# Performance work log

Hardware: AMD Instinct MI355X
Metric: run time of the kernel (lower is better)

Reference implementation:

```python
import jax, jax.numpy as jnp
import numpy as np
import math

N_FUNC = 32
LR_START, LR_DECAY = 1.0, 0.977
WEIGHT_DECAY, AMP_DECAY, MM_LR = 0.01, 0.01, 0.03
N_SAMP, BATCH, MOMENTUM = 32, 16, 0.85
N_FEAT, N_TARGET, MEM_SIZE = 1024, 512, 16384
DATA_SIZE = 100
SQRT_NF = math.sqrt(N_FUNC)


def setup_inputs() -> dict:
    key = jax.random.key(0)
    ks = jax.random.split(key, 16)
    p = jnp.linspace(0.01, 0.99, N_FUNC)[:, None]
    center_freq = jnp.log(p / (1.0 - p))  # logit of linspace, as in __init__
    return {
        "t": DATA_SIZE,
        "data_size": DATA_SIZE,
        "ts": jax.random.randint(ks[0], (N_SAMP,), 0, DATA_SIZE + 1),
        "x": jax.random.normal(ks[1], (N_FEAT,), jnp.float32),
        "z": jax.random.normal(ks[2], (N_TARGET,), jnp.float32),
        "memory": jax.random.normal(ks[3], (MEM_SIZE, N_TARGET), jnp.float32),
        "t_memory": jax.random.randint(ks[4], (MEM_SIZE,), 0, DATA_SIZE),
        "feat_memory": jax.random.normal(ks[5], (MEM_SIZE, N_FEAT), jnp.float32),
        "amp_re": 1.0 / SQRT_NF + 0.01 * jax.random.normal(ks[6], (N_FUNC, N_TARGET), jnp.float32),
        "amp_im": 0.01 * jax.random.normal(ks[7], (N_FUNC, N_TARGET), jnp.float32),
        "freq": 0.1 * jax.random.normal(ks[8], (N_FUNC, 1), jnp.float32),
        "center_freq": center_freq.astype(jnp.float32),
        "res_proj": 0.02 * jax.random.normal(ks[9], (N_FEAT + N_TARGET, N_TARGET), jnp.float32),
        "feat_mean": 0.1 * jax.random.normal(ks[10], (N_FEAT,), jnp.float32),
        "bias": 0.1 * jax.random.normal(ks[11], (N_TARGET,), jnp.float32),
        "amp_grad_re": 0.01 * jax.random.normal(ks[12], (N_FUNC, N_TARGET), jnp.float32),
        "amp_grad_im": 0.01 * jax.random.normal(ks[13], (N_FUNC, N_TARGET), jnp.float32),
        "freq_grad": 0.01 * jax.random.normal(ks[14], (N_FUNC, 1), jnp.float32),
        "res_proj_grad": 0.001 * jax.random.normal(ks[15], (N_FEAT + N_TARGET, N_TARGET), jnp.float32),
    }


def _get_freq(freq, center_freq):
    fr = center_freq + jnp.tanh(freq) * (64.0 / N_FUNC)
    return jax.nn.sigmoid(fr) * 0.5


def _evaluate(t, amp_re, amp_im, freq, bias, center_freq):
    # t: [B]; amp: [F, T]; freq/center_freq: [F, 1]
    fr = _get_freq(freq, center_freq)                      # [F, 1]
    ph = (2.0 * math.pi) * t[:, None, None] * fr           # [B, F, 1]
    # Re(exp(i*ph) * (amp_re + i*amp_im)) = cos*amp_re - sin*amp_im
    z = (jnp.cos(ph) * amp_re - jnp.sin(ph) * amp_im).sum(1) / SQRT_NF
    return z + bias                                        # [B, T]


def _get_resid(x, z, res_proj, feat_mean, bias):
    r = jnp.concatenate([x - feat_mean, z - bias], axis=-1) @ res_proj
    return r / (jnp.abs(r) + 1.0)


def reference(t, data_size, ts, x, z, memory, t_memory, feat_memory,
              amp_re, amp_im, freq, center_freq, res_proj, feat_mean, bias,
              amp_grad_re, amp_grad_im, freq_grad, res_proj_grad):
    # scatter new sample into the ring buffers
    memory = memory.at[data_size].set(z)
    feat_memory = feat_memory.at[data_size].set(x)
    t_memory = t_memory.at[data_size].set(t)
    ds_new = data_size + 1
    lr = LR_START * LR_DECAY ** ds_new  # lr after this call's decay
    # running means (torch uses the already-incremented data_size)
    bias = (bias * ds_new + z) / (ds_new + 1)
    feat_mean = (feat_mean * ds_new + x) / (ds_new + 1)

    for b in range(N_SAMP // BATCH):
        batch = ts[b * BATCH:(b + 1) * BATCH]
        t_b = t_memory[batch].astype(jnp.float32)
        z_b = memory[batch]
        x_b = feat_memory[batch]

        def loss_fn(a_re, a_im, fq, rp):
            z_ = _evaluate(t_b, a_re, a_im, fq, bias, center_freq)
            amp_abs = jnp.sqrt(a_re ** 2 + a_im ** 2)
            loss = jnp.sqrt(amp_abs).sum() * AMP_DECAY
            loss = loss + jnp.abs(z_b - z_).sum(-1).mean()
            resid = _get_resid(x_b, z_, rp, feat_mean, bias)
            z2 = jax.lax.stop_gradient(z_) + resid
            res_loss = jnp.abs(z_b - z2).sum(-1).mean()
            # torch uses self.res_proj (buffer) here -> no grad through this term
            res_loss = res_loss + jnp.abs(jax.lax.stop_gradient(rp)).sum() * WEIGHT_DECAY
            return loss + res_loss * MM_LR

        ag_re, ag_im, fg, rg = jax.grad(loss_fn, argnums=(0, 1, 2, 3))(amp_re, amp_im, freq, res_proj)
        # momentum decay then normalized-grad accumulate, then SGD step
        anorm = jnp.sqrt((ag_re ** 2).sum() + (ag_im ** 2).sum()) + 1.0  # complex vector norm
        amp_grad_re = amp_grad_re * MOMENTUM + ag_re / anorm
        amp_grad_im = amp_grad_im * MOMENTUM + ag_im / anorm
        amp_re = amp_re - amp_grad_re * lr
        amp_im = amp_im - amp_grad_im * lr
        fnorm = jnp.sqrt((fg ** 2).sum()) + 1.0
        freq_grad = freq_grad * MOMENTUM + fg / fnorm
        freq = freq - freq_grad * lr
        rnorm = jnp.sqrt((rg ** 2).sum()) + 1.0
        res_proj_grad = res_proj_grad * MOMENTUM + rg / rnorm
        res_proj = res_proj - res_proj_grad * lr

    return (memory, t_memory, feat_memory, amp_re, amp_im, freq, res_proj,
            bias, feat_mean, amp_grad_re, amp_grad_im, freq_grad, res_proj_grad)
```

## Files before the change

### kernel.cpp

```cpp
#include <hip/hip_runtime.h>
#include <hip/hip_cooperative_groups.h>
#include <math.h>

namespace cg = cooperative_groups;

#define NT 512
#define NF 1024
#define NFUNC 32
#define BATCHSZ 16

typedef float v4f __attribute__((ext_vector_type(4)));
typedef int   v4i __attribute__((ext_vector_type(4)));

constexpr int O_MEM  = 0;
constexpr int O_TMEM = 8388608;
constexpr int O_FEAT = 8404992;
constexpr int O_ARE  = 25182208;
constexpr int O_AIM  = 25198592;
constexpr int O_FREQ = 25214976;
constexpr int O_RP   = 25215008;
constexpr int O_BIAS = 26001440;
constexpr int O_FM   = 26001952;
constexpr int O_AGR  = 26002976;
constexpr int O_AGI  = 26019360;
constexpr int O_FGR  = 26035744;
constexpr int O_RPG  = 26035776;

constexpr int W_LR    = 0;
constexpr int W_ANORM = 2;
constexpr int W_RNORM = 4;
constexpr int W_GFR   = 8;
constexpr int W_TB    = 72;
constexpr int W_C     = 96;
constexpr int W_S     = 608;
constexpr int W_CATZ  = 1120;
constexpr int W_CATX  = 9312;
constexpr int W_GR    = 25696;
constexpr int W_G     = 33888;
constexpr int W_AGRE  = 42080;
constexpr int W_AGIM  = 58464;
constexpr int W_RPART = 74848;

constexpr float MM_LR = 0.03f;
constexpr float AMP_DECAY = 0.01f;
constexpr float MOM = 0.85f;
constexpr float INV_SQRT_NF = 0.17677669529663687f;
constexpr float TWO_PI = 6.283185307179586f;

constexpr int NB = 512;
constexpr int CHUNK = 786944;
constexpr int NCOPY = 256;

constexpr int R_MEM_END  = 2097152;
constexpr int R_FEAT_END = 6291456;

struct KParams {
    const int *t, *dsp, *ts;
    const float *x, *z, *memory;
    const int *t_memory;
    const float *feat_memory;
    const float *amp_re, *amp_im, *freq, *cf, *res_proj, *feat_mean, *bias;
    const float *amp_grad_re, *amp_grad_im, *freq_grad, *res_proj_grad;
    float *out, *ws;
};

__device__ __forceinline__ float sgnf(float x) {
    return (x > 0.f) ? 1.f : ((x < 0.f) ? -1.f : 0.f);
}

__device__ __forceinline__ float wave_reduce(float v) {
#pragma unroll
    for (int o = 32; o > 0; o >>= 1) v += __shfl_down(v, o, 64);
    return v;
}

__device__ __forceinline__ void copy_span(int tg, int nthr, int cbase, int cend,
    int dsv, int tt,
    const float* __restrict__ x, const float* __restrict__ z,
    const float* __restrict__ memory, const int* __restrict__ t_memory,
    const float* __restrict__ feat_memory, float* __restrict__ out)
{
    {
        const int a1 = cend < R_MEM_END ? cend : R_MEM_END;
        const v4f* __restrict__ src = (const v4f*)memory;
        const v4f* __restrict__ zz  = (const v4f*)z;
        v4f* __restrict__ dst = (v4f*)(out + O_MEM);
        int u = cbase + tg;
        for (; u + nthr < a1; u += 2 * nthr) {
            const int u1 = u + nthr;
            v4f v0 = __builtin_nontemporal_load((u  >> 7) == dsv ? zz + (u  & 127) : src + u );
            v4f v1 = __builtin_nontemporal_load((u1 >> 7) == dsv ? zz + (u1 & 127) : src + u1);
            __builtin_nontemporal_store(v0, dst + u );
            __builtin_nontemporal_store(v1, dst + u1);
        }
        for (; u < a1; u += nthr) {
            v4f v = __builtin_nontemporal_load((u >> 7) == dsv ? zz + (u & 127) : src + u);
            __builtin_nontemporal_store(v, dst + u);
        }
    }
    {
        const int a0 = cbase > R_MEM_END ? cbase : R_MEM_END;
        const int a1 = cend < R_FEAT_END ? cend : R_FEAT_END;
        const v4f* __restrict__ src = (const v4f*)feat_memory;
        const v4f* __restrict__ xx  = (const v4f*)x;
        v4f* __restrict__ dst = (v4f*)(out + O_FEAT);
        int u = a0 + tg;
        for (; u + nthr < a1; u += 2 * nthr) {
            const int u1 = u + nthr;
            const int f0 = u - R_MEM_END, f1 = u1 - R_MEM_END;
            v4f v0 = __builtin_nontemporal_load((f0 >> 8) == dsv ? xx + (f0 & 255) : src + f0);
            v4f v1 = __builtin_nontemporal_load((f1 >> 8) == dsv ? xx + (f1 & 255) : src + f1);
            __builtin_nontemporal_store(v0, dst + f0);
            __builtin_nontemporal_store(v1, dst + f1);
        }
        for (; u < a1; u += nthr) {
            const int f = u - R_MEM_END;
            v4f v = __builtin_nontemporal_load((f >> 8) == dsv ? xx + (f & 255) : src + f);
            __builtin_nontemporal_store(v, dst + f);
        }
    }
    {
        const int a0 = cbase > R_FEAT_END ? cbase : R_FEAT_END;
        const int a1 = cend;
        if (a1 > a0) {
            const float ft = (float)tt;
            const v4i* __restrict__ tm = (const v4i*)t_memory;
            v4f* __restrict__ dst = (v4f*)(out + O_TMEM);
            for (int u = a0 + tg; u < a1; u += nthr) {
                const int f = u - R_FEAT_END;
                const v4i iv = __builtin_nontemporal_load(tm + f);
                const int e = f * 4;
                v4f v;
                v.x = (e + 0 == dsv) ? ft : (float)iv.x;
                v.y = (e + 1 == dsv) ? ft : (float)iv.y;
                v.z = (e + 2 == dsv) ? ft : (float)iv.z;
                v.w = (e + 3 == dsv) ? ft : (float)iv.w;
                __builtin_nontemporal_store(v, dst + f);
            }
        }
    }
}

__global__ __launch_bounds__(256, 2) void k_fused(KParams p)
{
    cg::grid_group grid = cg::this_grid();
    const int bidx = (int)blockIdx.x;
    const int tid  = (int)threadIdx.x;

    __shared__ float c_l[32], s_l[32], cat[96];
    __shared__ float g_sh[NT], d_sh[NT];
    __shared__ float red[4];

    float* __restrict__ out = p.out;
    float* __restrict__ ws  = p.ws;
    const int dsv = *p.dsp;
    const int tt  = *p.t;
    const float nn = (float)(dsv + 1), dd = (float)(dsv + 2);
    const int tg   = bidx * 256 + tid;
    const int nthr = NB * 256;

    for (int b = 0; b < 2; ++b) {
        const float* __restrict__ are_src = b ? out + O_ARE : p.amp_re;
        const float* __restrict__ aim_src = b ? out + O_AIM : p.amp_im;
        const float* __restrict__ fq_src  = b ? out + O_FREQ: p.freq;
        const float* __restrict__ rp_src  = b ? out + O_RP  : p.res_proj;
        const float* __restrict__ agr_src = b ? out + O_AGR : p.amp_grad_re;
        const float* __restrict__ agi_src = b ? out + O_AGI : p.amp_grad_im;
        const float* __restrict__ fgr_src = b ? out + O_FGR : p.freq_grad;
        const float* __restrict__ rpg_src = b ? out + O_RPG : p.res_proj_grad;

        if (bidx < 256) {
            const int i = bidx >> 4, s = bidx & 15;
            const int bi = p.ts[b * BATCHSZ + i];
            if (tid < 32) {
                float f  = fq_src[tid];
                float th = tanhf(f);
                float u  = p.cf[tid] + 2.f * th;
                float sg = 1.f / (1.f + expf(-u));
                float fr = 0.5f * sg;
                float tb = (bi == dsv) ? (float)tt : (float)p.t_memory[bi];
                float ph = TWO_PI * tb * fr;
                float cv = cosf(ph), sv = sinf(ph);
                c_l[tid] = cv; s_l[tid] = sv;
                if (s == 0) {
                    ws[W_C + i*32 + tid] = cv; ws[W_S + i*32 + tid] = sv;
                    if (tid == 0) ws[W_TB + i] = tb;
                }
            }
            if (bidx == 0) {
                if (tid == 64) ws[W_ANORM + b] = 0.f;
                if (tid == 65) ws[W_RNORM + b] = 0.f;
                if (tid == 66 && b == 0) ws[W_LR] = (float)pow(0.977, (double)(dsv + 1));
                if (tid >= 96 && tid < 128) ws[W_GFR + b*32 + tid - 96] = 0.f;
            }
            __syncthreads();
            if (tid < 96) {
                int pe = s * 96 + tid;
                float cv;
                if (pe < NF) {
                    float fmv = (p.feat_mean[pe] * nn + p.x[pe]) / dd;
                    float xv  = (bi == dsv) ? p.x[pe] : p.feat_memory[bi*NF + pe];
                    cv = xv - fmv;
                    ws[W_CATX + i*NF + pe] = cv;
                } else {
                    int q = pe - NF;
                    float acc = 0.f;
#pragma unroll
                    for (int k = 0; k < 32; ++k)
                        acc += c_l[k] * are_src[k*NT + q] - s_l[k] * aim_src[k*NT + q];
                    cv = acc * INV_SQRT_NF;
                    ws[W_CATZ + i*NT + q] = cv;
                }
                cat[tid] = cv;
            }
            __syncthreads();
            const int j = tid;
            const float* rpb = rp_src + (size_t)s * 96 * NT;
            float a0 = 0.f, a1 = 0.f, b0 = 0.f, b1 = 0.f;
#pragma unroll 8
            for (int pp = 0; pp < 96; pp += 2) {
                float c0 = cat[pp], c1 = cat[pp + 1];
                a0 += c0 * rpb[pp*NT + j];
                a1 += c0 * rpb[pp*NT + j + 256];
                b0 += c1 * rpb[(pp+1)*NT + j];
                b1 += c1 * rpb[(pp+1)*NT + j + 256];
            }
            ws[W_RPART + s*8192 + i*NT + j]       = a0 + b0;
            ws[W_RPART + s*8192 + i*NT + j + 256] = a1 + b1;
        }
        {
            int cb = (b*4 + 0) * CHUNK;
            copy_span(tg, nthr, cb, cb + CHUNK, dsv, tt, p.x, p.z, p.memory, p.t_memory, p.feat_memory, out);
        }
        __threadfence();
        grid.sync();
        __threadfence();

        for (int vb = bidx; vb < 1024; vb += NB) {
            const int i = vb >> 6, jg = vb & 63;
            const int bi = p.ts[b * BATCHSZ + i];
#pragma unroll
            for (int ll = 0; ll < 2; ++ll) {
                int l = tid + ll * 256;
                float r = 0.f;
#pragma unroll
                for (int s = 0; s < 16; ++s) r += ws[W_RPART + s*8192 + i*NT + l];
                float bn = (p.bias[l] * nn + p.z[l]) / dd;
                float zj = ws[W_CATZ + i*NT + l] + bn;
                float zb = (bi == dsv) ? p.z[l] : p.memory[bi*NT + l];
                float s1 = sgnf(zj - zb);
                float ar = fabsf(r) + 1.f;
                float z2 = zj + r / ar;
                float g  = sgnf(z2 - zb) * (MM_LR / 16.f) / (ar * ar);
                g_sh[l] = g; d_sh[l] = s1 * (1.f / 16.f);
                if (jg == 0) {
                    ws[W_GR + i*NT + l] = g;
                    if (b == 0 && i == 0) out[O_BIAS + l] = bn;
                }
            }
            if (b == 0 && jg == 0 && i < 2) {
#pragma unroll
                for (int ll = 0; ll < 2; ++ll) {
                    int pe = i * 512 + tid + ll * 256;
                    out[O_FM + pe] = (p.feat_mean[pe] * nn + p.x[pe]) / dd;
                }
            }
            __syncthreads();
            const int w = tid >> 6, lane = tid & 63;
#pragma unroll
            for (int jj = 0; jj < 2; ++jj) {
                int j = jg * 8 + w * 2 + jj;
                const float* rrow = rp_src + (size_t)(NF + j) * NT;
                float acc = 0.f;
#pragma unroll
                for (int l = lane; l < NT; l += 64) acc += g_sh[l] * rrow[l];
                acc = wave_reduce(acc);
                if (lane == 0) ws[W_G + i*NT + j] = d_sh[j] + acc;
            }
            __syncthreads();
        }
        {
            int cb = (b*4 + 1) * CHUNK;
            copy_span(tg, nthr, cb, cb + CHUNK, dsv, tt, p.x, p.z, p.memory, p.t_memory, p.feat_memory, out);
        }
        __threadfence();
        grid.sync();
        __threadfence();

        for (int it = bidx; it < 3264; it += NB) {
            if (it < 64) {
                int e = it*256 + tid;
                int k = e >> 9;
                float gre = 0.f, gim = 0.f;
#pragma unroll
                for (int i2 = 0; i2 < 16; ++i2) {
                    float G = ws[W_G + i2*NT + (e & 511)];
                    gre += G * ws[W_C + i2*32 + k];
                    gim += G * ws[W_S + i2*32 + k];
                }
                float re = are_src[e], im = aim_src[e];
                float aa = sqrtf(re*re + im*im);
                float dec = AMP_DECAY / (2.f * aa * sqrtf(aa));
                float agr =  gre * INV_SQRT_NF + re * dec;
                float agi = -gim * INV_SQRT_NF + im * dec;
                ws[W_AGRE + e] = agr;
                ws[W_AGIM + e] = agi;
                float v = wave_reduce(agr*agr + agi*agi);
                if ((tid & 63) == 0) red[tid >> 6] = v;
                __syncthreads();
                if (tid == 0) atomicAdd(&ws[W_ANORM + b], red[0]+red[1]+red[2]+red[3]);
            } else if (it < 192) {
                int wid = tid >> 6, lane = tid & 63;
                int pair = (it - 64)*4 + wid;
                int i = pair >> 5, k = pair & 31;
                float ck = ws[W_C + i*32 + k], sk = ws[W_S + i*32 + k];
                float acc = 0.f;
#pragma unroll
                for (int j = lane; j < NT; j += 64)
                    acc += ws[W_G + i*NT + j] * (-sk * are_src[k*NT + j] - ck * aim_src[k*NT + j]);
                acc = wave_reduce(acc);
                if (lane == 0)
                    atomicAdd(&ws[W_GFR + b*32 + k], acc * TWO_PI * ws[W_TB + i] * INV_SQRT_NF);
            } else {
                int e = (it - 192)*256 + tid;
                int pr = e >> 9, j = e & 511;
                float rg = 0.f;
#pragma unroll
                for (int i2 = 0; i2 < 16; ++i2) {
                    float cv = (pr < NF) ? ws[W_CATX + i2*NF + pr]
                                         : ws[W_CATZ + i2*NT + (pr - NF)];
                    rg += cv * ws[W_GR + i2*NT + j];
                }
                float v = wave_reduce(rg * rg);
                if ((tid & 63) == 0) red[tid >> 6] = v;
                __syncthreads();
                if (tid == 0) atomicAdd(&ws[W_RNORM + b], red[0]+red[1]+red[2]+red[3]);
            }
            __syncthreads();
        }
        {
            int cb = (b*4 + 2) * CHUNK;
            copy_span(tg, nthr, cb, cb + CHUNK, dsv, tt, p.x, p.z, p.memory, p.t_memory, p.feat_memory, out);
        }
        __threadfence();
        grid.sync();
        __threadfence();

        const float lr = ws[W_LR];
        for (int it = bidx; it < 3137; it += NB) {
            if (it < 64) {
                int e = it*256 + tid;
                float anorm = sqrtf(ws[W_ANORM + b]) + 1.f;
                float mr = agr_src[e]*MOM + ws[W_AGRE + e]/anorm;
                out[O_AGR + e] = mr; out[O_ARE + e] = are_src[e] - mr*lr;
                float mi = agi_src[e]*MOM + ws[W_AGIM + e]/anorm;
                out[O_AGI + e] = mi; out[O_AIM + e] = aim_src[e] - mi*lr;
            } else if (it == 64) {
                if (tid < 64) {
                    float fg = 0.f, th = 0.f;
                    if (tid < 32) {
                        float f = fq_src[tid];
                        th = tanhf(f);
                        float u  = p.cf[tid] + 2.f*th;
                        float sg = 1.f / (1.f + expf(-u));
                        fg = ws[W_GFR + b*32 + tid] * sg*(1.f-sg)*(1.f-th*th);
                    }
                    float t2 = fg*fg;
#pragma unroll
                    for (int o = 32; o > 0; o >>= 1) t2 += __shfl_down(t2, o, 64);
                    float tot = __shfl(t2, 0, 64);
                    if (tid < 32) {
                        float fnorm = sqrtf(tot) + 1.f;
                        float m = fgr_src[tid]*MOM + fg/fnorm;
                        out[O_FGR + tid] = m;
                        out[O_FREQ + tid] = fq_src[tid] - m*lr;
                    }
                }
            } else {
                int e = (it - 65)*256 + tid;
                int pr = e >> 9, j = e & 511;
                float rg = 0.f;
#pragma unroll
                for (int i2 = 0; i2 < 16; ++i2) {
                    float cv = (pr < NF) ? ws[W_CATX + i2*NF + pr]
                                         : ws[W_CATZ + i2*NT + (pr - NF)];
                    rg += cv * ws[W_GR + i2*NT + j];
                }
                float rnorm = sqrtf(ws[W_RNORM + b]) + 1.f;
                float m = rpg_src[e]*MOM + rg/rnorm;
                out[O_RPG + e] = m; out[O_RP + e] = rp_src[e] - m*lr;
            }
        }
        {
            int cb = (b*4 + 3) * CHUNK;
            copy_span(tg, nthr, cb, cb + CHUNK, dsv, tt, p.x, p.z, p.memory, p.t_memory, p.feat_memory, out);
        }
        if (b == 0) { __threadfence(); grid.sync(); __threadfence(); }
    }
}

__device__ __forceinline__ void copy_role(int rb, int cbase, int ccnt,
    const int* __restrict__ tptr, const int* __restrict__ dsptr,
    const float* __restrict__ x, const float* __restrict__ z,
    const float* __restrict__ memory, const int* __restrict__ t_memory,
    const float* __restrict__ feat_memory, float* __restrict__ out)
{
    const int dsv = *dsptr;
    const int tt  = *tptr;
    copy_span(rb * 256 + (int)threadIdx.x, NCOPY * 256, cbase, cbase + ccnt,
              dsv, tt, x, z, memory, t_memory, feat_memory, out);
}

#define COPY_ARGS const int* __restrict__ tptr, const int* __restrict__ dsptr,            \
                  const float* __restrict__ x, const float* __restrict__ z,               \
                  const float* __restrict__ memory, const int* __restrict__ t_memory,     \
                  const float* __restrict__ feat_memory, int cbase, int ccnt
#define COPY_PASS tptr, dsptr, x, z, memory, t_memory, feat_memory

__global__ __launch_bounds__(256) void k_fwd_ab(int b, const int* __restrict__ ts,
    const float* __restrict__ cf,
    const float* __restrict__ are_src, const float* __restrict__ aim_src,
    const float* __restrict__ fq_src, const float* __restrict__ fm_in,
    const float* __restrict__ rp_src,
    float* __restrict__ out, float* __restrict__ ws, COPY_ARGS)
{
    int bb = blockIdx.x;
    const int tid = threadIdx.x;
    if (bb < NCOPY) { copy_role(bb, cbase, ccnt, COPY_PASS, out); return; }
    bb -= NCOPY;
    const int i = bb >> 4, s = bb & 15;
    __shared__ float c_l[32], s_l[32], cat[96];
    const int dsv = *dsptr;
    const int bi = ts[b * BATCHSZ + i];
    if (tid < 32) {
        float f  = fq_src[tid];
        float th = tanhf(f);
        float u  = cf[tid] + 2.f * th;
        float sg = 1.f / (1.f + expf(-u));
        float fr = 0.5f * sg;
        float tb = (bi == dsv) ? (float)(*tptr) : (float)t_memory[bi];
        float ph = TWO_PI * tb * fr;
        float cv = cosf(ph), sv = sinf(ph);
        c_l[tid] = cv; s_l[tid] = sv;
        if (s == 0) {
            ws[W_C + i*32 + tid] = cv; ws[W_S + i*32 + tid] = sv;
            if (tid == 0) ws[W_TB + i] = tb;
        }
    }
    if (bb == 0) {
        if (tid == 64) ws[W_ANORM + b] = 0.f;
        if (tid == 65) ws[W_RNORM + b] = 0.f;
        if (tid == 66 && b == 0) ws[W_LR] = (float)pow(0.977, (double)(dsv + 1));
        if (tid >= 96 && tid < 128) ws[W_GFR + b*32 + tid - 96] = 0.f;
    }
    __syncthreads();
    if (tid < 96) {
        int p = s * 96 + tid;
        float cv;
        if (p < NF) {
            const float nn = (float)(dsv + 1), dd = (float)(dsv + 2);
            float fmv = (fm_in[p] * nn + x[p]) / dd;
            float xv  = (bi == dsv) ? x[p] : feat_memory[bi*NF + p];
            cv = xv - fmv;
            ws[W_CATX + i*NF + p] = cv;
        } else {
            int q = p - NF;
            float acc = 0.f;
#pragma unroll
            for (int k = 0; k < 32; ++k)
                acc += c_l[k] * are_src[k*NT + q] - s_l[k] * aim_src[k*NT + q];
            cv = acc * INV_SQRT_NF;
            ws[W_CATZ + i*NT + q] = cv;
        }
        cat[tid] = cv;
    }
    __syncthreads();
    const int j = tid;
    const float* rpb = rp_src + (size_t)s * 96 * NT;
    float a0 = 0.f, a1 = 0.f, b0 = 0.f, b1 = 0.f;
#pragma unroll 8
    for (int p = 0; p < 96; p += 2) {
        float c0 = cat[p], c1 = cat[p + 1];
        a0 += c0 * rpb[p*NT + j];
        a1 += c0 * rpb[p*NT + j + 256];
        b0 += c1 * rpb[(p+1)*NT + j];
        b1 += c1 * rpb[(p+1)*NT + j + 256];
    }
    ws[W_RPART + s*8192 + i*NT + j]       = a0 + b0;
    ws[W_RPART + s*8192 + i*NT + j + 256] = a1 + b1;
}

__global__ __launch_bounds__(256) void k_eplg3(int b, const int* __restrict__ ts,
    const float* __restrict__ bias_in, const float* __restrict__ fm_in,
    const float* __restrict__ rp_src,
    float* __restrict__ out, float* __restrict__ ws, COPY_ARGS)
{
    int bb = blockIdx.x;
    const int tid = threadIdx.x;
    if (bb < NCOPY) { copy_role(bb, cbase, ccnt, COPY_PASS, out); return; }
    bb -= NCOPY;
    const int i = bb >> 6, jg = bb & 63;
    __shared__ float g_sh[NT], d_sh[NT];
    const int dsv = *dsptr;
    const int bi = ts[b * BATCHSZ + i];
    const float nn = (float)(dsv + 1), dd = (float)(dsv + 2);
#pragma unroll
    for (int ll = 0; ll < 2; ++ll) {
        int l = tid + ll * 256;
        float r = 0.f;
#pragma unroll
        for (int s = 0; s < 16; ++s) r += ws[W_RPART + s*8192 + i*NT + l];
        float bn = (bias_in[l] * nn + z[l]) / dd;
        float zj = ws[W_CATZ + i*NT + l] + bn;
        float zb = (bi == dsv) ? z[l] : memory[bi*NT + l];
        float s1 = sgnf(zj - zb);
        float ar = fabsf(r) + 1.f;
        float z2 = zj + r / ar;
        float g  = sgnf(z2 - zb) * (MM_LR / 16.f) / (ar * ar);
        g_sh[l] = g; d_sh[l] = s1 * (1.f / 16.f);
        if (jg == 0) {
            ws[W_GR + i*NT + l] = g;
            if (b == 0 && i == 0) out[O_BIAS + l] = bn;
        }
    }
    if (b == 0 && jg == 0 && i < 2) {
#pragma unroll
        for (int ll = 0; ll < 2; ++ll) {
            int p = i * 512 + tid + ll * 256;
            out[O_FM + p] = (fm_in[p] * nn + x[p]) / dd;
        }
    }
    __syncthreads();
    const int w = tid >> 6, lane = tid & 63;
#pragma unroll
    for (int jj = 0; jj < 2; ++jj) {
        int j = jg * 8 + w * 2 + jj;
        const float* rrow = rp_src + (size_t)(NF + j) * NT;
        float acc = 0.f;
#pragma unroll
        for (int l = lane; l < NT; l += 64) acc += g_sh[l] * rrow[l];
        acc = wave_reduce(acc);
        if (lane == 0) ws[W_G + i*NT + j] = d_sh[j] + acc;
    }
}

__global__ __launch_bounds__(256) void k_norms(int b,
    const float* __restrict__ are_src, const float* __restrict__ aim_src,
    float* __restrict__ out, float* __restrict__ ws, COPY_ARGS)
{
    __shared__ float red[4];
    int bb = blockIdx.x;
    const int tid = threadIdx.x;
    if (bb < NCOPY) { copy_role(bb, cbase, ccnt, COPY_PASS, out); return; }
    bb -= NCOPY;
    if (bb < 64) {
        int e = bb*256 + tid;
        int k = e >> 9;
        float gre = 0.f, gim = 0.f;
#pragma unroll
        for (int i2 = 0; i2 < 16; ++i2) {
            float G = ws[W_G + i2*NT + (e & 511)];
            gre += G * ws[W_C + i2*32 + k];
            gim += G * ws[W_S + i2*32 + k];
        }
        float re = are_src[e], im = aim_src[e];
        float aa = sqrtf(re*re + im*im);
        float dec = AMP_DECAY / (2.f * aa * sqrtf(aa));
        float agr =  gre * INV_SQRT_NF + re * dec;
        float agi = -gim * INV_SQRT_NF + im * dec;
        ws[W_AGRE + e] = agr;
        ws[W_AGIM + e] = agi;
        float v = wave_reduce(agr*agr + agi*agi);
        if ((tid & 63) == 0) red[tid >> 6] = v;
        __syncthreads();
        if (tid == 0) atomicAdd(&ws[W_ANORM + b], red[0]+red[1]+red[2]+red[3]);
    } else if (bb < 192) {
        int wid = tid >> 6, lane = tid & 63;
        int pair = (bb - 64)*4 + wid;
        int i = pair >> 5, k = pair & 31;
        float ck = ws[W_C + i*32 + k], sk = ws[W_S + i*32 + k];
        float acc = 0.f;
#pragma unroll
        for (int j = lane; j < NT; j += 64)
            acc += ws[W_G + i*NT + j] * (-sk * are_src[k*NT + j] - ck * aim_src[k*NT + j]);
        acc = wave_reduce(acc);
        if (lane == 0)
            atomicAdd(&ws[W_GFR + b*32 + k], acc * TWO_PI * ws[W_TB + i] * INV_SQRT_NF);
    } else {
        int e = (bb - 192)*256 + tid;
        int p = e >> 9, j = e & 511;
        float rg = 0.f;
#pragma unroll
        for (int i2 = 0; i2 < 16; ++i2) {
            float cat = (p < NF) ? ws[W_CATX + i2*NF + p]
                                 : ws[W_CATZ + i2*NT + (p - NF)];
            rg += cat * ws[W_GR + i2*NT + j];
        }
        float v = wave_reduce(rg * rg);
        if ((tid & 63) == 0) red[tid >> 6] = v;
        __syncthreads();
        if (tid == 0) atomicAdd(&ws[W_RNORM + b], red[0]+red[1]+red[2]+red[3]);
    }
}

__global__ __launch_bounds__(256) void k_upd(int b, const float* __restrict__ cf,
    const float* __restrict__ are_src, const float* __restrict__ aim_src,
    const float* __restrict__ agr_src, const float* __restrict__ agi_src,
    const float* __restrict__ fq_src,  const float* __restrict__ fgr_src,
    const float* __restrict__ rp_src,  const float* __restrict__ rpg_src,
    float* __restrict__ out, float* __restrict__ ws, COPY_ARGS)
{
    int bb = blockIdx.x;
    const int tid = threadIdx.x;
    if (bb < NCOPY) { copy_role(bb, cbase, ccnt, COPY_PASS, out); return; }
    bb -= NCOPY;
    const float lr = ws[W_LR];
    if (bb < 64) {
        int e = bb*256 + tid;
        float anorm = sqrtf(ws[W_ANORM + b]) + 1.f;
        float mr = agr_src[e]*MOM + ws[W_AGRE + e]/anorm;
        out[O_AGR + e] = mr; out[O_ARE + e] = are_src[e] - mr*lr;
        float mi = agi_src[e]*MOM + ws[W_AGIM + e]/anorm;
        out[O_AGI + e] = mi; out[O_AIM + e] = aim_src[e] - mi*lr;
    } else if (bb == 64) {
        if (tid < 64) {
            float fg = 0.f, th = 0.f;
            if (tid < 32) {
                float f = fq_src[tid];
                th = tanhf(f);
                float u  = cf[tid] + 2.f*th;
                float sg = 1.f / (1.f + expf(-u));
                fg = ws[W_GFR + b*32 + tid] * sg*(1.f-sg)*(1.f-th*th);
            }
            float t2 = fg*fg;
#pragma unroll
            for (int o = 32; o > 0; o >>= 1) t2 += __shfl_down(t2, o, 64);
            float tot = __shfl(t2, 0, 64);
            if (tid < 32) {
                float fnorm = sqrtf(tot) + 1.f;
                float m = fgr_src[tid]*MOM + fg/fnorm;
                out[O_FGR + tid] = m;
                out[O_FREQ + tid] = fq_src[tid] - m*lr;
            }
        }
    } else {
        int e = (bb - 65)*256 + tid;
        int p = e >> 9, j = e & 511;
        float rg = 0.f;
#pragma unroll
        for (int i2 = 0; i2 < 16; ++i2) {
            float cat = (p < NF) ? ws[W_CATX + i2*NF + p]
                                 : ws[W_CATZ + i2*NT + (p - NF)];
            rg += cat * ws[W_GR + i2*NT + j];
        }
        float rnorm = sqrtf(ws[W_RNORM + b]) + 1.f;
        float m = rpg_src[e]*MOM + rg/rnorm;
        out[O_RPG + e] = m; out[O_RP + e] = rp_src[e] - m*lr;
    }
}

extern "C" void kernel_launch(void* const* d_in, const int* in_sizes, int n_in,
                              void* d_out, int out_size, void* d_ws, size_t ws_size,
                              hipStream_t stream)
{
    const int*   t            = (const int*)d_in[0];
    const int*   dsp          = (const int*)d_in[1];
    const int*   ts           = (const int*)d_in[2];
    const float* x            = (const float*)d_in[3];
    const float* z            = (const float*)d_in[4];
    const float* memory       = (const float*)d_in[5];
    const int*   t_memory     = (const int*)d_in[6];
    const float* feat_memory  = (const float*)d_in[7];
    const float* amp_re       = (const float*)d_in[8];
    const float* amp_im       = (const float*)d_in[9];
    const float* freq         = (const float*)d_in[10];
    const float* cf           = (const float*)d_in[11];
    const float* res_proj     = (const float*)d_in[12];
    const float* feat_mean    = (const float*)d_in[13];
    const float* bias         = (const float*)d_in[14];
    const float* amp_grad_re  = (const float*)d_in[15];
    const float* amp_grad_im  = (const float*)d_in[16];
    const float* freq_grad    = (const float*)d_in[17];
    const float* res_proj_grad= (const float*)d_in[18];
    float* out = (float*)d_out;
    float* ws  = (float*)d_ws;

    static int coop_ok = -1;
    if (coop_ok < 0) {
        int dev = 0;
        hipGetDevice(&dev);
        hipDeviceProp_t prop;
        int ok = (hipGetDeviceProperties(&prop, dev) == hipSuccess);
        int maxb = 0;
        if (ok) ok = (hipOccupancyMaxActiveBlocksPerMultiprocessor(&maxb, k_fused, 256, 0) == hipSuccess);
        coop_ok = (ok && prop.cooperativeLaunch &&
                   (long long)maxb * prop.multiProcessorCount >= NB) ? 1 : 0;
    }

    if (coop_ok == 1) {
        KParams p;
        p.t = t; p.dsp = dsp; p.ts = ts; p.x = x; p.z = z; p.memory = memory;
        p.t_memory = t_memory; p.feat_memory = feat_memory;
        p.amp_re = amp_re; p.amp_im = amp_im; p.freq = freq; p.cf = cf;
        p.res_proj = res_proj; p.feat_mean = feat_mean; p.bias = bias;
        p.amp_grad_re = amp_grad_re; p.amp_grad_im = amp_grad_im;
        p.freq_grad = freq_grad; p.res_proj_grad = res_proj_grad;
        p.out = out; p.ws = ws;
        void* args[] = { (void*)&p };
        hipError_t e = hipLaunchCooperativeKernel(reinterpret_cast<void*>(k_fused),
                                                  dim3(NB), dim3(256), args, 0, stream);
        if (e == hipSuccess) return;
        coop_ok = 0;
    }

    const float* ARE[2] = { amp_re,        out + O_ARE };
    const float* AIM[2] = { amp_im,        out + O_AIM };
    const float* AGR[2] = { amp_grad_re,   out + O_AGR };
    const float* AGI[2] = { amp_grad_im,   out + O_AGI };
    const float* FQ [2] = { freq,          out + O_FREQ };
    const float* FGR[2] = { freq_grad,     out + O_FGR };
    const float* RP [2] = { res_proj,      out + O_RP };
    const float* RPG[2] = { res_proj_grad, out + O_RPG };

    const int per = 786944;
    int base = 0;
    auto nxt = [&](int& cb, int& cc) { cb = base; cc = per; base += cc; };
    int cb, cc;
    for (int b = 0; b < 2; ++b) {
        nxt(cb, cc);
        k_fwd_ab<<<256 + NCOPY, 256, 0, stream>>>(b, ts, cf, ARE[b], AIM[b], FQ[b],
            feat_mean, RP[b], out, ws, t, dsp, x, z, memory, t_memory, feat_memory, cb, cc);
        nxt(cb, cc);
        k_eplg3<<<1024 + NCOPY, 256, 0, stream>>>(b, ts, bias, feat_mean, RP[b], out, ws,
            t, dsp, x, z, memory, t_memory, feat_memory, cb, cc);
        nxt(cb, cc);
        k_norms<<<3264 + NCOPY, 256, 0, stream>>>(b, ARE[b], AIM[b], out, ws,
            t, dsp, x, z, memory, t_memory, feat_memory, cb, cc);
        nxt(cb, cc);
        k_upd<<<3137 + NCOPY, 256, 0, stream>>>(b, cf, ARE[b], AIM[b], AGR[b], AGI[b],
            FQ[b], FGR[b], RP[b], RPG[b], out, ws,
            t, dsp, x, z, memory, t_memory, feat_memory, cb, cc);
    }
}
```

Baseline: 329.3 us.

## Replace cooperative grid sync with atomic counter barrier and double grid size

Removes the cooperative-groups launch and grid.sync. Each grid barrier becomes a single-use atomic counter in workspace that thread 0 of every block increments and then spins on with s_sleep. The counters are zeroed by a memset on the stream before each launch. The grid doubles to 1024 blocks with launch bounds raised to 4 blocks per CU, adding parallelism to the copy and compute loops. Forward progress now relies on all blocks being co-resident, which is only checked through an occupancy query rather than guaranteed by a cooperative launch, so the barrier could deadlock. The extra memset adds a small launch cost.

```diff
diff --git a/kernel.cpp b/kernel.cpp
--- a/kernel.cpp
+++ b/kernel.cpp
@@ -1,8 +1,5 @@
 #include <hip/hip_runtime.h>
-#include <hip/hip_cooperative_groups.h>
 #include <math.h>
-
-namespace cg = cooperative_groups;
 
 #define NT 512
 #define NF 1024
@@ -31,6 +28,7 @@
 constexpr int W_RNORM = 4;
 constexpr int W_GFR   = 8;
 constexpr int W_TB    = 72;
+constexpr int W_BARU  = 88;
 constexpr int W_C     = 96;
 constexpr int W_S     = 608;
 constexpr int W_CATZ  = 1120;
@@ -47,7 +45,7 @@
 constexpr float INV_SQRT_NF = 0.17677669529663687f;
 constexpr float TWO_PI = 6.283185307179586f;
 
-constexpr int NB = 512;
+constexpr int NB = 1024;
 constexpr int CHUNK = 786944;
 constexpr int NCOPY = 256;
 
@@ -72,6 +70,17 @@
 #pragma unroll
     for (int o = 32; o > 0; o >>= 1) v += __shfl_down(v, o, 64);
     return v;
+}
+
+__device__ __forceinline__ void gbar(unsigned* c, unsigned nb) {
+    __syncthreads();
+    __threadfence();
+    if (threadIdx.x == 0) {
+        __hip_atomic_fetch_add(c, 1u, __ATOMIC_ACQ_REL, __HIP_MEMORY_SCOPE_AGENT);
+        while (__hip_atomic_load(c, __ATOMIC_ACQUIRE, __HIP_MEMORY_SCOPE_AGENT) < nb)
+            __builtin_amdgcn_s_sleep(8);
+    }
+    __syncthreads();
 }
 
 __device__ __forceinline__ void copy_span(int tg, int nthr, int cbase, int cend,
@@ -141,9 +150,8 @@
     }
 }
 
-__global__ __launch_bounds__(256, 2) void k_fused(KParams p)
+__global__ __launch_bounds__(256, 4) void k_fused2(KParams p)
 {
-    cg::grid_group grid = cg::this_grid();
     const int bidx = (int)blockIdx.x;
     const int tid  = (int)threadIdx.x;
 
@@ -153,6 +161,8 @@
 
     float* __restrict__ out = p.out;
     float* __restrict__ ws  = p.ws;
+    unsigned* bars = (unsigned*)(ws + W_BARU);
+    int bs = 0;
     const int dsv = *p.dsp;
     const int tt  = *p.t;
     const float nn = (float)(dsv + 1), dd = (float)(dsv + 2);
@@ -232,9 +242,7 @@
             int cb = (b*4 + 0) * CHUNK;
             copy_span(tg, nthr, cb, cb + CHUNK, dsv, tt, p.x, p.z, p.memory, p.t_memory, p.feat_memory, out);
         }
-        __threadfence();
-        grid.sync();
-        __threadfence();
+        gbar(&bars[bs++], NB);
 
         for (int vb = bidx; vb < 1024; vb += NB) {
             const int i = vb >> 6, jg = vb & 63;
@@ -283,9 +291,7 @@
             int cb = (b*4 + 1) * CHUNK;
             copy_span(tg, nthr, cb, cb + CHUNK, dsv, tt, p.x, p.z, p.memory, p.t_memory, p.feat_memory, out);
         }
-        __threadfence();
-        grid.sync();
-        __threadfence();
+        gbar(&bars[bs++], NB);
 
         for (int it = bidx; it < 3264; it += NB) {
             if (it < 64) {
@@ -342,9 +348,7 @@
             int cb = (b*4 + 2) * CHUNK;
             copy_span(tg, nthr, cb, cb + CHUNK, dsv, tt, p.x, p.z, p.memory, p.t_memory, p.feat_memory, out);
         }
-        __threadfence();
-        grid.sync();
-        __threadfence();
+        gbar(&bars[bs++], NB);
 
         const float lr = ws[W_LR];
         for (int it = bidx; it < 3137; it += NB) {
@@ -395,7 +399,7 @@
             int cb = (b*4 + 3) * CHUNK;
             copy_span(tg, nthr, cb, cb + CHUNK, dsv, tt, p.x, p.z, p.memory, p.t_memory, p.feat_memory, out);
         }
-        if (b == 0) { __threadfence(); grid.sync(); __threadfence(); }
+        if (b == 0) gbar(&bars[bs++], NB);
     }
 }
 
@@ -685,19 +689,20 @@
     float* out = (float*)d_out;
     float* ws  = (float*)d_ws;
 
-    static int coop_ok = -1;
-    if (coop_ok < 0) {
+    int fused_ok = 0;
+    {
         int dev = 0;
-        hipGetDevice(&dev);
-        hipDeviceProp_t prop;
-        int ok = (hipGetDeviceProperties(&prop, dev) == hipSuccess);
-        int maxb = 0;
-        if (ok) ok = (hipOccupancyMaxActiveBlocksPerMultiprocessor(&maxb, k_fused, 256, 0) == hipSuccess);
-        coop_ok = (ok && prop.cooperativeLaunch &&
-                   (long long)maxb * prop.multiProcessorCount >= NB) ? 1 : 0;
-    }
-
-    if (coop_ok == 1) {
+        if (hipGetDevice(&dev) == hipSuccess) {
+            hipDeviceProp_t prop;
+            int maxb = 0;
+            if (hipGetDeviceProperties(&prop, dev) == hipSuccess &&
+                hipOccupancyMaxActiveBlocksPerMultiprocessor(&maxb, k_fused2, 256, 0) == hipSuccess)
+                fused_ok = ((long long)maxb * prop.multiProcessorCount >= NB) ? 1 : 0;
+        }
+    }
+
+    if (fused_ok) {
+        hipMemsetAsync((void*)(ws + W_BARU), 0, 8 * sizeof(unsigned), stream);
         KParams p;
         p.t = t; p.dsp = dsp; p.ts = ts; p.x = x; p.z = z; p.memory = memory;
         p.t_memory = t_memory; p.feat_memory = feat_memory;
@@ -706,11 +711,8 @@
         p.amp_grad_re = amp_grad_re; p.amp_grad_im = amp_grad_im;
         p.freq_grad = freq_grad; p.res_proj_grad = res_proj_grad;
         p.out = out; p.ws = ws;
-        void* args[] = { (void*)&p };
-        hipError_t e = hipLaunchCooperativeKernel(reinterpret_cast<void*>(k_fused),
-                                                  dim3(NB), dim3(256), args, 0, stream);
-        if (e == hipSuccess) return;
-        coop_ok = 0;
+        k_fused2<<<NB, 256, 0, stream>>>(p);
+        return;
     }
 
     const float* ARE[2] = { amp_re,        out + O_ARE };
```

Measured after the change: 328.6 us. About the same (-0.2%).
